# Performance work log

Measured on AMD Instinct MI355X. Metric: run time of the kernel, lower is better.

The kernel has to match this reference:

```python
import jax, jax.numpy as jnp
import numpy as np

D_MODEL = 2048
HQ = 32
HK = 8
DK = D_MODEL // HQ  # 64
G = HQ // HK        # 4
VOCAB = 32000
B, S = 1, 2048


def setup_inputs() -> dict:
    key = jax.random.key(0)
    ks = jax.random.split(key, 7)
    scale = 1.0 / np.sqrt(D_MODEL)
    X = jax.random.randint(ks[0], (B, S), 0, VOCAB, dtype=jnp.int64)
    emb = jax.random.normal(ks[1], (VOCAB, D_MODEL), dtype=jnp.float32)
    Wk = jax.random.normal(ks[2], (HK * DK, D_MODEL), dtype=jnp.float32) * scale
    Wv = jax.random.normal(ks[3], (HK * DK, D_MODEL), dtype=jnp.float32) * scale
    Wq = jax.random.normal(ks[4], (D_MODEL, D_MODEL), dtype=jnp.float32) * scale
    Wo_w = jax.random.normal(ks[5], (D_MODEL, D_MODEL), dtype=jnp.float32) * scale
    Wo_b = jax.random.normal(ks[6], (D_MODEL,), dtype=jnp.float32) * scale
    return {"X": X, "emb": emb, "Wk": Wk, "Wv": Wv, "Wq": Wq, "Wo_w": Wo_w, "Wo_b": Wo_b}


def reference(X, emb, Wk, Wv, Wq, Wo_w, Wo_b):
    e = emb[X]  # [B,S,D]
    b, s, _ = e.shape
    # torch Linear: y = x @ W.T (weights stored [out,in])
    k = (e @ Wk.T).reshape(b, s, HK, DK)            # [B,S,Hk,dk]
    v = (e @ Wv.T).reshape(b, s, HK, DK)            # [B,S,Hk,dk]
    q = (e @ Wq.T).reshape(b, s, HK, G, DK)         # q head index = i*G + g
    # scores: [B,Hk,G,S,S] — same math as expanding KV to Hq heads, no copy
    scores = jnp.einsum('bsigd,btid->bigst', q, k) / jnp.sqrt(jnp.asarray(DK, e.dtype))
    w = jax.nn.softmax(scores, axis=-1)
    ctx = jnp.einsum('bigst,btid->bsigd', w, v).reshape(b, s, D_MODEL)
    return ctx @ Wo_w.T + Wo_b
```

## Files before the change

### kernel.cpp

```cpp
#include <hip/hip_runtime.h>


typedef __bf16 bf16x8 __attribute__((ext_vector_type(8)));
typedef float f32x4 __attribute__((ext_vector_type(4)));
typedef float f32x16 __attribute__((ext_vector_type(16)));
typedef unsigned short ushort8_t __attribute__((ext_vector_type(8)));
typedef unsigned int uint4_t __attribute__((ext_vector_type(4)));

#define DEVI static __device__ __forceinline__

#define QSCALE 0.180336880111112f

DEVI unsigned short f2bf(float f) {
    union { float f; unsigned int u; } c; c.f = f;
    unsigned int u = c.u;
    unsigned int r = (u + 0x7FFFu + ((u >> 16) & 1u)) >> 16;
    return (unsigned short)r;
}

DEVI f32x4 mfma16(bf16x8 a, bf16x8 b, f32x4 c) {
    return __builtin_amdgcn_mfma_f32_16x16x32_bf16(a, b, c, 0, 0, 0);
}
DEVI f32x16 mfma32(bf16x8 a, bf16x8 b, f32x16 c) {
    return __builtin_amdgcn_mfma_f32_32x32x16_bf16(a, b, c, 0, 0, 0);
}
DEVI unsigned cvtpk(float a, float b) {
    unsigned r;
    asm("v_cvt_pk_bf16_f32 %0, %1, %2" : "=v"(r) : "v"(a), "v"(b));
    return r;
}
DEVI void plswap(unsigned& a, unsigned& b) {
    asm("v_permlane32_swap_b32 %0, %1" : "+v"(a), "+v"(b));
}
DEVI float exp2r(float x) {
#if __has_builtin(__builtin_amdgcn_exp2f)
    return __builtin_amdgcn_exp2f(x);
#else
    float r;
    asm("v_exp_f32 %0, %1\n\ts_nop 1" : "=v"(r) : "v"(x));
    return r;
#endif
}
DEVI void gload16(const unsigned short* g, unsigned short* l) {
    __builtin_amdgcn_global_load_lds(
        (const __attribute__((address_space(1))) void*)g,
        (__attribute__((address_space(3))) void*)l, 16, 0, 0);
}
#define WAIT_VM(n) asm volatile("s_waitcnt vmcnt(" #n ")" ::: "memory")
#define WAIT_LGKM0() asm volatile("s_waitcnt lgkmcnt(0)" ::: "memory")
#define BAR() __builtin_amdgcn_s_barrier()

DEVI void cvt8(const float* src, unsigned short* dst) {
    float4 f0 = *(const float4*)(src);
    float4 f1 = *(const float4*)(src + 4);
    ushort8_t v;
    v[0] = f2bf(f0.x); v[1] = f2bf(f0.y); v[2] = f2bf(f0.z); v[3] = f2bf(f0.w);
    v[4] = f2bf(f1.x); v[5] = f2bf(f1.y); v[6] = f2bf(f1.z); v[7] = f2bf(f1.w);
    *(ushort8_t*)(dst) = v;
}

__global__ __launch_bounds__(256)
void prep_k(const int* __restrict__ X, const float* __restrict__ emb,
            unsigned short* __restrict__ e,
            const float* __restrict__ Wk, unsigned short* __restrict__ Wkb,
            const float* __restrict__ Wv, unsigned short* __restrict__ Wvb,
            const float* __restrict__ Wq, unsigned short* __restrict__ Wqb,
            const float* __restrict__ Wo, unsigned short* __restrict__ Wob) {
    int b = blockIdx.x;
    if (b < 2048) {
        long long row = X[b];
        cvt8(emb + row * 2048 + threadIdx.x * 8, e + (size_t)b * 2048 + threadIdx.x * 8);
        return;
    }
    b -= 2048;
    const float* s; unsigned short* d; int off;
    if (b < 512) { s = Wk; d = Wkb; off = b; }
    else if (b < 1024) { s = Wv; d = Wvb; off = b - 512; }
    else if (b < 3072) { s = Wq; d = Wqb; off = b - 1024; }
    else { s = Wo; d = Wob; off = b - 3072; }
    size_t idx = ((size_t)off * 256 + threadIdx.x) * 8;
    cvt8(s + idx, d + idx);
}

template<int OM0, int OM1, int OM2, int BUFS>
__global__ __launch_bounds__(256)
void gemm_swz_k(const unsigned short* __restrict__ A,
                const unsigned short* __restrict__ W0, const unsigned short* __restrict__ W1,
                const unsigned short* __restrict__ W2,
                void* __restrict__ C0, void* __restrict__ C1, void* __restrict__ C2,
                int t1, int t2, int ldc0, int ldc1, int ldc2,
                const float* __restrict__ bias) {
    __shared__ unsigned short As[BUFS * 128 * 64];
    __shared__ unsigned short Bs[BUFS * 128 * 64];
    const int cpx = gridDim.x >> 3;
    int id = blockIdx.x;
    int swz = (id & 7) * cpx + (id >> 3);
    const int bx = swz & 15;
    const int by = swz >> 4;
    const unsigned short* Wp; void* Cp; int ldc, om, nb;
    if (by < t1)      { Wp = W0; Cp = C0; ldc = ldc0; om = OM0; nb = by; }
    else if (by < t2) { Wp = W1; Cp = C1; ldc = ldc1; om = OM1; nb = by - t1; }
    else              { Wp = W2; Cp = C2; ldc = ldc2; om = OM2; nb = by - t2; }
    const int m0 = bx * 128, n0 = nb * 128;
    const int tid = threadIdx.x, lane = tid & 63, w = tid >> 6;
    const int wm = (w >> 1) * 64, wn = (w & 1) * 64;
    const int lr = lane & 15, lg = lane >> 4;
    const int srow = tid >> 3, sj = tid & 7;

    f32x4 acc[4][4];
    #pragma unroll
    for (int i = 0; i < 4; i++)
        #pragma unroll
        for (int j = 0; j < 4; j++) acc[i][j] = {};

    #define G_STAGE(buf, k0)                                                          \
        _Pragma("unroll")                                                             \
        for (int i = 0; i < 4; i++) {                                                 \
            int row = srow + i * 32;                                                  \
            int jj = sj ^ (row & 7);                                                  \
            unsigned short* ad = As + (buf) * 8192 + (w * 64 + i * 256) * 8;          \
            unsigned short* bd = Bs + (buf) * 8192 + (w * 64 + i * 256) * 8;          \
            gload16(A  + (size_t)(m0 + row) * 2048 + (k0) + jj * 8, ad);              \
            gload16(Wp + (size_t)(n0 + row) * 2048 + (k0) + jj * 8, bd);              \
        }

    #define G_COMPUTE(bC)                                                             \
    {                                                                                 \
        const unsigned short* Asb = As + (bC) * 8192;                                 \
        const unsigned short* Bsb = Bs + (bC) * 8192;                                 \
        _Pragma("unroll")                                                             \
        for (int kk = 0; kk < 2; kk++) {                                              \
            bf16x8 af[4], bfr[4];                                                     \
            _Pragma("unroll")                                                         \
            for (int mi = 0; mi < 4; mi++) {                                          \
                int r = wm + mi * 16 + lr;                                            \
                int g = (kk * 4 + lg) ^ (r & 7);                                      \
                af[mi] = *(const bf16x8*)(&Asb[r * 64 + g * 8]);                      \
            }                                                                         \
            _Pragma("unroll")                                                         \
            for (int ni = 0; ni < 4; ni++) {                                          \
                int r = wn + ni * 16 + lr;                                            \
                int g = (kk * 4 + lg) ^ (r & 7);                                      \
                bfr[ni] = *(const bf16x8*)(&Bsb[r * 64 + g * 8]);                     \
            }                                                                         \
            __builtin_amdgcn_s_setprio(1);                                            \
            _Pragma("unroll")                                                         \
            for (int mi = 0; mi < 4; mi++)                                            \
                _Pragma("unroll")                                                     \
                for (int ni = 0; ni < 4; ni++)                                        \
                    acc[mi][ni] = mfma16(af[mi], bfr[ni], acc[mi][ni]);               \
            __builtin_amdgcn_s_setprio(0);                                            \
        }                                                                             \
    }

    if constexpr (BUFS == 2) {
        G_STAGE(0, 0);
        for (int s = 0; s < 32; ++s) {
            const int cur = s & 1;
            if (s < 31) {
                G_STAGE(cur ^ 1, (s + 1) * 64);
                WAIT_VM(8);
            } else {
                WAIT_VM(0);
            }
            BAR();
            G_COMPUTE(cur);
            WAIT_LGKM0();
            BAR();
        }
    } else {
        G_STAGE(0, 0);
        G_STAGE(1, 64);
        int bC = 0, bS = 2;
        for (int s = 0; s < 32; ++s) {
            if (s < 30) {
                WAIT_VM(8);
            } else {
                WAIT_VM(0);
            }
            BAR();
            if (s < 30) G_STAGE(bS, (s + 2) * 64);
            G_COMPUTE(bC);
            bC = (bC == 2) ? 0 : bC + 1;
            bS = (bS == 2) ? 0 : bS + 1;
        }
    }
    #undef G_COMPUTE
    #undef G_STAGE

    #pragma unroll
    for (int mi = 0; mi < 4; mi++)
        #pragma unroll
        for (int ni = 0; ni < 4; ni++) {
            int col = n0 + wn + ni * 16 + lr;
            #pragma unroll
            for (int jj = 0; jj < 4; jj++) {
                int rowg = m0 + wm + mi * 16 + lg * 4 + jj;
                float vv = acc[mi][ni][jj];
                if (om == 0) {
                    ((unsigned short*)Cp)[(size_t)rowg * ldc + col] = f2bf(vv);
                } else if (om == 1) {
                    ((float*)Cp)[(size_t)rowg * ldc + col] = vv + bias[col];
                } else if (om == 2) {
                    ((unsigned short*)Cp)[(size_t)col * ldc + rowg] = f2bf(vv);
                } else {
                    ((unsigned short*)Cp)[(size_t)rowg * ldc + col] = f2bf(vv * QSCALE);
                }
            }
        }
}

__global__ __launch_bounds__(256)
void attn2_k(const unsigned short* __restrict__ Qb, const unsigned short* __restrict__ Kb,
             const unsigned short* __restrict__ VbT, unsigned short* __restrict__ Ctx) {
    __shared__ unsigned short Ks[3 * 64 * 64];
    __shared__ unsigned short Vts[3 * 64 * 64];
    int id = blockIdx.x;
    int swz = (id & 7) * 64 + (id >> 3);
    const int hq = swz >> 4;
    const int qt = swz & 15;
    const int ikv = hq >> 2;
    const int tid = threadIdx.x, lane = tid & 63, w = tid >> 6;
    const int l31 = lane & 31, hi = lane >> 5;
    const int qrow = qt * 128 + w * 32 + l31;
    const int srow = tid >> 3, sj = tid & 7;

    bf16x8 qf[4];
    #pragma unroll
    for (int ks = 0; ks < 4; ks++)
        qf[ks] = *(const bf16x8*)(Qb + (size_t)qrow * 2048 + hq * 64 + ks * 16 + hi * 8);

    int ko0[4], ko1[4];
    #pragma unroll
    for (int ks = 0; ks < 4; ks++) {
        int gr = (2 * ks + hi) ^ (l31 & 7);
        ko0[ks] = l31 * 64 + gr * 8;
        ko1[ks] = (32 + l31) * 64 + gr * 8;
    }

    f32x16 oacc0 = {}, oacc1 = {};
    float rsa0 = 0.f, rsa1 = 0.f, rsa2 = 0.f, rsa3 = 0.f;

    #define A_STAGE(buf, t0)                                                          \
        _Pragma("unroll")                                                             \
        for (int i = 0; i < 2; i++) {                                                 \
            int row = srow + i * 32;                                                  \
            int jj = sj ^ (row & 7);                                                  \
            unsigned short* kd = Ks + (buf) * 4096 + (w * 64 + i * 256) * 8;          \
            unsigned short* vd = Vts + (buf) * 4096 + (w * 64 + i * 256) * 8;         \
            gload16(Kb + (size_t)((t0) + row) * 512 + ikv * 64 + jj * 8, kd);         \
            gload16(VbT + (size_t)(ikv * 64 + row) * 2048 + (t0) + jj * 8, vd);       \
        }

    #define BODY(t, CB, SB, DO_STAGE, LAST)                                           \
    {                                                                                 \
        if (LAST) { WAIT_VM(0); } else { WAIT_VM(4); }                                \
        BAR();                                                                        \
        if (DO_STAGE) A_STAGE(SB, ((t) + 2) * 64);                                    \
        const unsigned short* Ksb = Ks + (CB) * 4096;                                 \
        const unsigned short* Vsb = Vts + (CB) * 4096;                                \
        f32x16 s0 = {}, s1 = {};                                                      \
        __builtin_amdgcn_s_setprio(1);                                                \
        _Pragma("unroll")                                                             \
        for (int ks = 0; ks < 4; ks++) {                                              \
            bf16x8 kf0 = *(const bf16x8*)(&Ksb[ko0[ks]]);                             \
            bf16x8 kf1 = *(const bf16x8*)(&Ksb[ko1[ks]]);                             \
            s0 = mfma32(kf0, qf[ks], s0);                                             \
            s1 = mfma32(kf1, qf[ks], s1);                                             \
        }                                                                             \
        __builtin_amdgcn_s_setprio(0);                                                \
        _Pragma("unroll")                                                             \
        for (int r = 0; r < 16; r += 4) {                                             \
            s0[r]     = exp2r(s0[r]);     rsa0 += s0[r];                              \
            s0[r + 1] = exp2r(s0[r + 1]); rsa1 += s0[r + 1];                          \
            s0[r + 2] = exp2r(s0[r + 2]); rsa2 += s0[r + 2];                          \
            s0[r + 3] = exp2r(s0[r + 3]); rsa3 += s0[r + 3];                          \
        }                                                                             \
        _Pragma("unroll")                                                             \
        for (int r = 0; r < 16; r += 4) {                                             \
            s1[r]     = exp2r(s1[r]);     rsa0 += s1[r];                              \
            s1[r + 1] = exp2r(s1[r + 1]); rsa1 += s1[r + 1];                          \
            s1[r + 2] = exp2r(s1[r + 2]); rsa2 += s1[r + 2];                          \
            s1[r + 3] = exp2r(s1[r + 3]); rsa3 += s1[r + 3];                          \
        }                                                                             \
        uint4_t pw[4];                                                                \
        _Pragma("unroll")                                                             \
        for (int c = 0; c < 2; c++) {                                                 \
            unsigned a   = cvtpk(s0[8 * c + 0], s0[8 * c + 1]);                       \
            unsigned bb  = cvtpk(s0[8 * c + 2], s0[8 * c + 3]);                       \
            unsigned cc2 = cvtpk(s0[8 * c + 4], s0[8 * c + 5]);                       \
            unsigned dd  = cvtpk(s0[8 * c + 6], s0[8 * c + 7]);                       \
            plswap(a, cc2); plswap(bb, dd);                                           \
            pw[c][0] = a; pw[c][1] = bb; pw[c][2] = cc2; pw[c][3] = dd;               \
        }                                                                             \
        _Pragma("unroll")                                                             \
        for (int c = 0; c < 2; c++) {                                                 \
            unsigned a   = cvtpk(s1[8 * c + 0], s1[8 * c + 1]);                       \
            unsigned bb  = cvtpk(s1[8 * c + 2], s1[8 * c + 3]);                       \
            unsigned cc2 = cvtpk(s1[8 * c + 4], s1[8 * c + 5]);                       \
            unsigned dd  = cvtpk(s1[8 * c + 6], s1[8 * c + 7]);                       \
            plswap(a, cc2); plswap(bb, dd);                                           \
            pw[2 + c][0] = a; pw[2 + c][1] = bb; pw[2 + c][2] = cc2; pw[2 + c][3] = dd; \
        }                                                                             \
        __builtin_amdgcn_s_setprio(1);                                                \
        _Pragma("unroll")                                                             \
        for (int ks = 0; ks < 4; ks++) {                                              \
            bf16x8 pa = __builtin_bit_cast(bf16x8, pw[ks]);                           \
            bf16x8 vf0 = *(const bf16x8*)(&Vsb[ko0[ks]]);                             \
            bf16x8 vf1 = *(const bf16x8*)(&Vsb[ko1[ks]]);                             \
            oacc0 = mfma32(pa, vf0, oacc0);                                           \
            oacc1 = mfma32(pa, vf1, oacc1);                                           \
        }                                                                             \
        __builtin_amdgcn_s_setprio(0);                                                \
    }

    A_STAGE(0, 0);
    A_STAGE(1, 64);
    for (int tt = 0; tt < 30; tt += 3) {
        BODY(tt,     0, 2, true, false);
        BODY(tt + 1, 1, 0, true, false);
        BODY(tt + 2, 2, 1, true, false);
    }
    BODY(30, 0, 0, false, false);
    BODY(31, 1, 0, false, true);
    #undef BODY
    #undef A_STAGE

    float rs = (rsa0 + rsa1) + (rsa2 + rsa3);
    rs += __shfl_xor(rs, 32, 64);
    float linv = 1.0f / rs;
    #pragma unroll
    for (int r = 0; r < 16; r++) {
        const int qp = (r & 3) + 8 * (r >> 2);
        float lv = __shfl(linv, qp + 4 * hi, 64);
        int row = qt * 128 + w * 32 + qp + 4 * hi;
        Ctx[(size_t)row * 2048 + hq * 64 + l31]      = f2bf(oacc0[r] * lv);
        Ctx[(size_t)row * 2048 + hq * 64 + 32 + l31] = f2bf(oacc1[r] * lv);
    }
}

extern "C" void kernel_launch(void* const* d_in, const int* in_sizes, int n_in,
                              void* d_out, int out_size, void* d_ws, size_t ws_size,
                              hipStream_t stream) {
    (void)in_sizes; (void)n_in; (void)out_size; (void)ws_size;
    const int*   X   = (const int*)d_in[0];
    const float* emb = (const float*)d_in[1];
    const float* Wk  = (const float*)d_in[2];
    const float* Wv  = (const float*)d_in[3];
    const float* Wq  = (const float*)d_in[4];
    const float* Wo  = (const float*)d_in[5];
    const float* Wb  = (const float*)d_in[6];

    unsigned short* e   = (unsigned short*)d_ws;
    unsigned short* Kb  = e   + (size_t)2048 * 2048;
    unsigned short* VbT = Kb  + (size_t)2048 * 512;
    unsigned short* Qb  = VbT + (size_t)512 * 2048;
    unsigned short* Ctx = Qb  + (size_t)2048 * 2048;
    unsigned short* Wkb = Ctx + (size_t)2048 * 2048;
    unsigned short* Wvb = Wkb + (size_t)512 * 2048;
    unsigned short* Wqb = Wvb + (size_t)512 * 2048;
    unsigned short* Wob = Wqb + (size_t)2048 * 2048;

    prep_k<<<dim3(2048 + 5120), dim3(256), 0, stream>>>(X, emb, e, Wk, Wkb, Wv, Wvb,
                                                        Wq, Wqb, Wo, Wob);
    gemm_swz_k<3, 0, 2, 2><<<dim3(384), dim3(256), 0, stream>>>(
        e, Wqb, Wkb, Wvb, (void*)Qb, (void*)Kb, (void*)VbT,
        16, 20, 2048, 512, 2048, nullptr);
    attn2_k<<<dim3(512), dim3(256), 0, stream>>>(Qb, Kb, VbT, Ctx);
    gemm_swz_k<1, 1, 1, 3><<<dim3(256), dim3(256), 0, stream>>>(
        Ctx, Wob, Wob, Wob, d_out, d_out, d_out,
        16, 32, 2048, 2048, 2048, Wb);
}
```

Measured before the change: 147.0 us.

## Double-buffer attention K/V tiles and split score blocks to raise occupancy

Cuts the attention kernel's shared-memory ring from three K/V stages to two and adds a launch-bounds hint of 4 blocks per CU. The two 32-row score blocks are now computed and exponentiated one after the other instead of together, which lowers peak register use. The aim is more resident waves per CU to hide latency. In exchange there is less prefetch depth and a second barrier per iteration, since the buffer must be drained before it is overwritten.

New measurement: 144.4 us. No clear change (-1.8%).

```diff
diff --git a/kernel.cpp b/kernel.cpp
--- a/kernel.cpp
+++ b/kernel.cpp
@@ -210,11 +210,11 @@
         }
 }
 
-__global__ __launch_bounds__(256)
+__global__ __launch_bounds__(256, 4)
 void attn2_k(const unsigned short* __restrict__ Qb, const unsigned short* __restrict__ Kb,
              const unsigned short* __restrict__ VbT, unsigned short* __restrict__ Ctx) {
-    __shared__ unsigned short Ks[3 * 64 * 64];
-    __shared__ unsigned short Vts[3 * 64 * 64];
+    __shared__ unsigned short Ks[2 * 64 * 64];
+    __shared__ unsigned short Vts[2 * 64 * 64];
     int id = blockIdx.x;
     int swz = (id & 7) * 64 + (id >> 3);
     const int hq = swz >> 4;
@@ -252,78 +252,85 @@
             gload16(VbT + (size_t)(ikv * 64 + row) * 2048 + (t0) + jj * 8, vd);       \
         }
 
-    #define BODY(t, CB, SB, DO_STAGE, LAST)                                           \
-    {                                                                                 \
-        if (LAST) { WAIT_VM(0); } else { WAIT_VM(4); }                                \
-        BAR();                                                                        \
-        if (DO_STAGE) A_STAGE(SB, ((t) + 2) * 64);                                    \
-        const unsigned short* Ksb = Ks + (CB) * 4096;                                 \
-        const unsigned short* Vsb = Vts + (CB) * 4096;                                \
-        f32x16 s0 = {}, s1 = {};                                                      \
-        __builtin_amdgcn_s_setprio(1);                                                \
-        _Pragma("unroll")                                                             \
-        for (int ks = 0; ks < 4; ks++) {                                              \
-            bf16x8 kf0 = *(const bf16x8*)(&Ksb[ko0[ks]]);                             \
-            bf16x8 kf1 = *(const bf16x8*)(&Ksb[ko1[ks]]);                             \
-            s0 = mfma32(kf0, qf[ks], s0);                                             \
-            s1 = mfma32(kf1, qf[ks], s1);                                             \
-        }                                                                             \
-        __builtin_amdgcn_s_setprio(0);                                                \
-        _Pragma("unroll")                                                             \
-        for (int r = 0; r < 16; r += 4) {                                             \
-            s0[r]     = exp2r(s0[r]);     rsa0 += s0[r];                              \
-            s0[r + 1] = exp2r(s0[r + 1]); rsa1 += s0[r + 1];                          \
-            s0[r + 2] = exp2r(s0[r + 2]); rsa2 += s0[r + 2];                          \
-            s0[r + 3] = exp2r(s0[r + 3]); rsa3 += s0[r + 3];                          \
-        }                                                                             \
-        _Pragma("unroll")                                                             \
-        for (int r = 0; r < 16; r += 4) {                                             \
-            s1[r]     = exp2r(s1[r]);     rsa0 += s1[r];                              \
-            s1[r + 1] = exp2r(s1[r + 1]); rsa1 += s1[r + 1];                          \
-            s1[r + 2] = exp2r(s1[r + 2]); rsa2 += s1[r + 2];                          \
-            s1[r + 3] = exp2r(s1[r + 3]); rsa3 += s1[r + 3];                          \
-        }                                                                             \
-        uint4_t pw[4];                                                                \
-        _Pragma("unroll")                                                             \
-        for (int c = 0; c < 2; c++) {                                                 \
-            unsigned a   = cvtpk(s0[8 * c + 0], s0[8 * c + 1]);                       \
-            unsigned bb  = cvtpk(s0[8 * c + 2], s0[8 * c + 3]);                       \
-            unsigned cc2 = cvtpk(s0[8 * c + 4], s0[8 * c + 5]);                       \
-            unsigned dd  = cvtpk(s0[8 * c + 6], s0[8 * c + 7]);                       \
-            plswap(a, cc2); plswap(bb, dd);                                           \
-            pw[c][0] = a; pw[c][1] = bb; pw[c][2] = cc2; pw[c][3] = dd;               \
-        }                                                                             \
-        _Pragma("unroll")                                                             \
-        for (int c = 0; c < 2; c++) {                                                 \
-            unsigned a   = cvtpk(s1[8 * c + 0], s1[8 * c + 1]);                       \
-            unsigned bb  = cvtpk(s1[8 * c + 2], s1[8 * c + 3]);                       \
-            unsigned cc2 = cvtpk(s1[8 * c + 4], s1[8 * c + 5]);                       \
-            unsigned dd  = cvtpk(s1[8 * c + 6], s1[8 * c + 7]);                       \
-            plswap(a, cc2); plswap(bb, dd);                                           \
-            pw[2 + c][0] = a; pw[2 + c][1] = bb; pw[2 + c][2] = cc2; pw[2 + c][3] = dd; \
-        }                                                                             \
-        __builtin_amdgcn_s_setprio(1);                                                \
-        _Pragma("unroll")                                                             \
-        for (int ks = 0; ks < 4; ks++) {                                              \
-            bf16x8 pa = __builtin_bit_cast(bf16x8, pw[ks]);                           \
-            bf16x8 vf0 = *(const bf16x8*)(&Vsb[ko0[ks]]);                             \
-            bf16x8 vf1 = *(const bf16x8*)(&Vsb[ko1[ks]]);                             \
-            oacc0 = mfma32(pa, vf0, oacc0);                                           \
-            oacc1 = mfma32(pa, vf1, oacc1);                                           \
-        }                                                                             \
-        __builtin_amdgcn_s_setprio(0);                                                \
-    }
-
     A_STAGE(0, 0);
-    A_STAGE(1, 64);
-    for (int tt = 0; tt < 30; tt += 3) {
-        BODY(tt,     0, 2, true, false);
-        BODY(tt + 1, 1, 0, true, false);
-        BODY(tt + 2, 2, 1, true, false);
-    }
-    BODY(30, 0, 0, false, false);
-    BODY(31, 1, 0, false, true);
-    #undef BODY
+    for (int t = 0; t < 32; ++t) {
+        const int cur = t & 1;
+        if (t < 31) {
+            A_STAGE(cur ^ 1, (t + 1) * 64);
+            WAIT_VM(4);
+        } else {
+            WAIT_VM(0);
+        }
+        BAR();
+        const unsigned short* Ksb = Ks + cur * 4096;
+        const unsigned short* Vsb = Vts + cur * 4096;
+
+        uint4_t pw[4];
+        {
+            f32x16 s = {};
+            __builtin_amdgcn_s_setprio(1);
+            #pragma unroll
+            for (int ks = 0; ks < 4; ks++) {
+                bf16x8 kf = *(const bf16x8*)(&Ksb[ko0[ks]]);
+                s = mfma32(kf, qf[ks], s);
+            }
+            __builtin_amdgcn_s_setprio(0);
+            #pragma unroll
+            for (int r = 0; r < 16; r += 4) {
+                s[r]     = exp2r(s[r]);     rsa0 += s[r];
+                s[r + 1] = exp2r(s[r + 1]); rsa1 += s[r + 1];
+                s[r + 2] = exp2r(s[r + 2]); rsa2 += s[r + 2];
+                s[r + 3] = exp2r(s[r + 3]); rsa3 += s[r + 3];
+            }
+            #pragma unroll
+            for (int c = 0; c < 2; c++) {
+                unsigned a   = cvtpk(s[8 * c + 0], s[8 * c + 1]);
+                unsigned bb  = cvtpk(s[8 * c + 2], s[8 * c + 3]);
+                unsigned cc2 = cvtpk(s[8 * c + 4], s[8 * c + 5]);
+                unsigned dd  = cvtpk(s[8 * c + 6], s[8 * c + 7]);
+                plswap(a, cc2); plswap(bb, dd);
+                pw[c][0] = a; pw[c][1] = bb; pw[c][2] = cc2; pw[c][3] = dd;
+            }
+        }
+        {
+            f32x16 s = {};
+            __builtin_amdgcn_s_setprio(1);
+            #pragma unroll
+            for (int ks = 0; ks < 4; ks++) {
+                bf16x8 kf = *(const bf16x8*)(&Ksb[ko1[ks]]);
+                s = mfma32(kf, qf[ks], s);
+            }
+            __builtin_amdgcn_s_setprio(0);
+            #pragma unroll
+            for (int r = 0; r < 16; r += 4) {
+                s[r]     = exp2r(s[r]);     rsa0 += s[r];
+                s[r + 1] = exp2r(s[r + 1]); rsa1 += s[r + 1];
+                s[r + 2] = exp2r(s[r + 2]); rsa2 += s[r + 2];
+                s[r + 3] = exp2r(s[r + 3]); rsa3 += s[r + 3];
+            }
+            #pragma unroll
+            for (int c = 0; c < 2; c++) {
+                unsigned a   = cvtpk(s[8 * c + 0], s[8 * c + 1]);
+                unsigned bb  = cvtpk(s[8 * c + 2], s[8 * c + 3]);
+                unsigned cc2 = cvtpk(s[8 * c + 4], s[8 * c + 5]);
+                unsigned dd  = cvtpk(s[8 * c + 6], s[8 * c + 7]);
+                plswap(a, cc2); plswap(bb, dd);
+                pw[2 + c][0] = a; pw[2 + c][1] = bb; pw[2 + c][2] = cc2; pw[2 + c][3] = dd;
+            }
+        }
+        __builtin_amdgcn_s_setprio(1);
+        #pragma unroll
+        for (int ks = 0; ks < 4; ks++) {
+            bf16x8 pa = __builtin_bit_cast(bf16x8, pw[ks]);
+            bf16x8 vf0 = *(const bf16x8*)(&Vsb[ko0[ks]]);
+            bf16x8 vf1 = *(const bf16x8*)(&Vsb[ko1[ks]]);
+            oacc0 = mfma32(pa, vf0, oacc0);
+            oacc1 = mfma32(pa, vf1, oacc1);
+        }
+        __builtin_amdgcn_s_setprio(0);
+        WAIT_LGKM0();
+        BAR();
+    }
     #undef A_STAGE
 
     float rs = (rsa0 + rsa1) + (rsa2 + rsa3);
```
